# Kernel optimization log

Hardware: AMD Instinct MI355X
Metric: run time of the kernel (lower is better)

Reference implementation:

```python
import jax, jax.numpy as jnp
import numpy as np


def setup_inputs() -> dict:
    key = jax.random.key(0)
    k1, k2, k3 = jax.random.split(key, 3)
    B, N, M, C = 4, 4096, 8192, 64
    PPU = 64.0  # points_per_unit
    xz = jax.random.normal(k1, (B, M, 1), dtype=jnp.float32) * 10.0  # grid locations
    z = jax.random.normal(k2, (B, C, M), dtype=jnp.float32)          # channels-first features
    x = jax.random.normal(k3, (B, N, 1), dtype=jnp.float32) * 10.0   # query locations
    log_scale = jnp.asarray(np.log(2.0 / PPU), dtype=jnp.float32)
    return {"xz": xz, "z": z, "x": x, "log_scale": log_scale}


def reference(xz, z, x, log_scale):
    # pairwise squared distances between x [B,N,1] and xz [B,M,1] -> [B,N,M]
    diff = x - jnp.swapaxes(xz, -1, -2)            # [B,N,M]
    dists2 = diff * diff
    # RBF weights (no normalization)
    weights = jnp.exp(-0.5 * dists2 / jnp.exp(2.0 * log_scale))  # [B,N,M]
    # z: [B,C,M] -> transpose -> [B,M,C]; weights @ z^T -> [B,N,C]
    out = jnp.einsum('bnm,bcm->bnc', weights, z)
    return out
```

## Files before the change

kernel.cpp:

```cpp
#include <hip/hip_runtime.h>
#include <math.h>

#define B 4
#define N 4096
#define M 8192
#define C 64
#define NB 2048
#define XMIN (-64.0f)
#define INV_BW 16.0f
#define CUT 10.0f
#define QG 16
#define NSUBP 4
#define NSUBQ 2

typedef __attribute__((ext_vector_type(8))) short short8;
typedef __attribute__((ext_vector_type(4))) float f32x4;

__device__ __forceinline__ int bucket_of(float v) {
    int k = (int)floorf((v - XMIN) * INV_BW);
    return min(max(k, 0), NB - 1);
}

__device__ __forceinline__ unsigned short f2bf(float f) {
    unsigned int u = __float_as_uint(f);
    return (unsigned short)((u + 0x7FFF + ((u >> 16) & 1)) >> 16);
}

__global__ __launch_bounds__(256) void hist_kernel(
    const float* __restrict__ xz, const float* __restrict__ x,
    int* __restrict__ part)
{
    const int t   = threadIdx.x;
    const int bid = blockIdx.x;
    __shared__ int h[NB];
    #pragma unroll
    for (int i = 0; i < 8; ++i) h[t + 256 * i] = 0;
    __syncthreads();

    const bool isQ = bid >= 16;
    const int  b   = isQ ? (bid - 16) >> 1 : bid >> 2;
    const int  sub = isQ ? (bid - 16) & 1  : bid & 3;
    const float* src = (isQ ? x + b * N : xz + b * M) + sub * 2048;

    #pragma unroll
    for (int j = 0; j < 2; ++j) {
        float4 v4 = *(const float4*)(src + t * 4 + j * 1024);
        atomicAdd(&h[bucket_of(v4.x)], 1);
        atomicAdd(&h[bucket_of(v4.y)], 1);
        atomicAdd(&h[bucket_of(v4.z)], 1);
        atomicAdd(&h[bucket_of(v4.w)], 1);
    }
    __syncthreads();
    #pragma unroll
    for (int i = 0; i < 8; ++i) part[bid * NB + t + 256 * i] = h[t + 256 * i];
}

__global__ __launch_bounds__(256) void scat_kernel(
    const float* __restrict__ xz, const float* __restrict__ x,
    const int* __restrict__ part,
    int* __restrict__ bucket_start,
    float* __restrict__ xs,
    int* __restrict__ islot,
    float* __restrict__ qcs,
    int* __restrict__ qis)
{
    const int t    = threadIdx.x;
    const int lane = t & 63;
    const int w    = t >> 6;
    const int bid  = blockIdx.x;
    const bool isQ = bid >= 16;
    const int  b   = isQ ? (bid - 16) >> 1 : bid >> 2;
    const int  sub = isQ ? (bid - 16) & 1  : bid & 3;
    const int  nsub = isQ ? NSUBQ : NSUBP;
    const int  pb0  = isQ ? 16 + b * 2 : b * 4;
    const float* src = (isQ ? x + b * N : xz + b * M) + sub * 2048;

    __shared__ int base[NB];
    __shared__ int cnt[NB];
    __shared__ int wsum[4];

    int tot[8], mine[8];
    #pragma unroll
    for (int j = 0; j < 8; ++j) { tot[j] = 0; mine[j] = 0; }
    for (int s_ = 0; s_ < nsub; ++s_) {
        #pragma unroll
        for (int j = 0; j < 8; ++j) {
            const int v = part[(pb0 + s_) * NB + t * 8 + j];
            tot[j] += v;
            if (s_ < sub) mine[j] += v;
        }
    }
    int pre[8]; int tsum = 0;
    #pragma unroll
    for (int j = 0; j < 8; ++j) { pre[j] = tsum; tsum += tot[j]; }
    int s = tsum;
    #pragma unroll
    for (int off = 1; off < 64; off <<= 1) {
        int up = __shfl_up(s, off, 64);
        if (lane >= off) s += up;
    }
    if (lane == 63) wsum[w] = s;
    #pragma unroll
    for (int i = 0; i < 8; ++i) cnt[t + 256 * i] = 0;
    __syncthreads();
    int woff = 0;
    for (int i = 0; i < w; ++i) woff += wsum[i];
    const int excl = woff + s - tsum;
    #pragma unroll
    for (int j = 0; j < 8; ++j) base[t * 8 + j] = excl + pre[j] + mine[j];
    if (!isQ && sub == 0) {
        #pragma unroll
        for (int j = 0; j < 8; ++j)
            bucket_start[b * (NB + 1) + t * 8 + j] = excl + pre[j];
        if (t == 255) bucket_start[b * (NB + 1) + NB] = woff + s;
    }
    __syncthreads();

    #pragma unroll
    for (int j = 0; j < 2; ++j) {
        float4 v4 = *(const float4*)(src + t * 4 + j * 1024);
        float vv[4] = {v4.x, v4.y, v4.z, v4.w};
        #pragma unroll
        for (int c = 0; c < 4; ++c) {
            const int k    = bucket_of(vv[c]);
            const int slot = base[k] + atomicAdd(&cnt[k], 1);
            const int orig = sub * 2048 + t * 4 + j * 1024 + c;
            if (!isQ) {
                xs[b * M + slot]    = vv[c];
                islot[b * M + orig] = slot;
            } else {
                qcs[b * N + slot] = vv[c];
                qis[b * N + slot] = orig;
            }
        }
    }
}

__global__ __launch_bounds__(1024) void permz_kernel(
    const float* __restrict__ z, const int* __restrict__ islot,
    unsigned short* __restrict__ zs)
{
    const int t  = threadIdx.x;
    const int b  = blockIdx.x >> 7;
    const int m0 = (blockIdx.x & 127) * 64;
    __shared__ float tile[64][65];
    __shared__ int slot_s[64];

    const int m = t & 63;
    #pragma unroll
    for (int k = 0; k < 4; ++k) {
        int c = (t >> 6) + 16 * k;
        tile[c][m] = z[((size_t)b * C + c) * M + m0 + m];
    }
    if (t < 64) slot_s[t] = islot[b * M + m0 + t];
    __syncthreads();

    const int j  = t >> 4;
    const int c4 = t & 15;
    ushort4 v4;
    v4.x = f2bf(tile[c4 * 4 + 0][j]);
    v4.y = f2bf(tile[c4 * 4 + 1][j]);
    v4.z = f2bf(tile[c4 * 4 + 2][j]);
    v4.w = f2bf(tile[c4 * 4 + 3][j]);
    ((ushort4*)zs)[((size_t)b * M + slot_s[j]) * 16 + c4] = v4;
}

__global__ __launch_bounds__(256) void gather_kernel(
    const float* __restrict__ log_scale,
    const int* __restrict__ bucket_start,
    const float* __restrict__ xs,
    const float* __restrict__ qcs,
    const int* __restrict__ qis,
    const unsigned short* __restrict__ zs,
    float* __restrict__ out)
{
    const int t    = threadIdx.x;
    const int lane = t & 63;
    const int w    = t >> 6;
    const int quad = lane >> 4;
    const int low4 = lane & 15;
    const int g  = blockIdx.x;
    const int b  = g >> 8;
    const int g0 = (g & 255) * QG;

    __shared__ unsigned short zr[64 * 64];
    __shared__ unsigned short wl[QG][72];
    __shared__ float qcS[QG];
    __shared__ int   qiS[QG];

    const float ls   = log_scale[0];
    const float coef = -0.5f * __expf(-2.0f * ls);
    const float R    = sqrtf(CUT / (-coef));

    if (t < QG) {
        qcS[t] = qcs[b * N + g0 + t];
        qiS[t] = qis[b * N + g0 + t];
    }
    __syncthreads();

    float xmin = qcS[0], xmax = qcS[0];
    #pragma unroll
    for (int j = 1; j < QG; ++j) {
        xmin = fminf(xmin, qcS[j]);
        xmax = fmaxf(xmax, qcS[j]);
    }
    const int s0 = bucket_start[b * (NB + 1) + bucket_of(xmin - R)];
    const int s1 = bucket_start[b * (NB + 1) + bucket_of(xmax + R) + 1];
    const int e0 = s0 & ~63;
    const int e1 = (s1 + 63) & ~63;

    const int qw = w * 4 + (lane >> 4);
    const int pg = lane & 15;
    const float qv = qcS[qw];

    f32x4 acc = {0.f, 0.f, 0.f, 0.f};

    const float* xsb = xs + b * M;
    const unsigned short* zsb = zs + (size_t)b * M * C;

    for (int cs = e0; cs < e1; cs += 64) {
        __syncthreads();
        #pragma unroll
        for (int r = 0; r < 2; ++r) {
            const unsigned short* gp =
                zsb + ((size_t)cs + (w * 2 + r) * 8 + (lane >> 3)) * C + (lane & 7) * 8;
            unsigned short* lp = zr + (w * 2 + r) * 512;
            __builtin_amdgcn_global_load_lds(
                (const __attribute__((address_space(1))) void*)gp,
                (__attribute__((address_space(3))) void*)lp, 16, 0, 0);
        }
        {
            const float4 xp4 = *(const float4*)(xsb + cs + pg * 4);
            float d0 = qv - xp4.x, d1 = qv - xp4.y;
            float d2 = qv - xp4.z, d3 = qv - xp4.w;
            ushort4 wv;
            wv.x = f2bf(__expf(coef * d0 * d0));
            wv.y = f2bf(__expf(coef * d1 * d1));
            wv.z = f2bf(__expf(coef * d2 * d2));
            wv.w = f2bf(__expf(coef * d3 * d3));
            *(ushort4*)&wl[qw][pg * 4] = wv;
        }
        __syncthreads();
        #pragma unroll
        for (int kh = 0; kh < 2; ++kh) {
            short8 afrag = *(const short8*)&wl[low4][kh * 32 + quad * 8];
            short8 bfrag;
            #pragma unroll
            for (int j = 0; j < 8; ++j) {
                const int p = kh * 32 + quad * 8 + j;
                bfrag[j] = (short)zr[p * 64 + w * 16 + low4];
            }
            acc = __builtin_amdgcn_mfma_f32_16x16x32_bf16(afrag, bfrag, acc, 0, 0, 0);
        }
    }

    #pragma unroll
    for (int r = 0; r < 4; ++r) {
        const int q = quad * 4 + r;
        out[((size_t)b * N + qiS[q]) * C + w * 16 + low4] = acc[r];
    }
}

extern "C" void kernel_launch(void* const* d_in, const int* in_sizes, int n_in,
                              void* d_out, int out_size, void* d_ws, size_t ws_size,
                              hipStream_t stream) {
    const float* xz = (const float*)d_in[0];
    const float* z  = (const float*)d_in[1];
    const float* x  = (const float*)d_in[2];
    const float* ls = (const float*)d_in[3];
    float* out = (float*)d_out;

    char* ws = (char*)d_ws;
    size_t off = 0;
    auto alloc = [&](size_t bytes) { void* p = ws + off; off += (bytes + 255) & ~size_t(255); return p; };

    unsigned short* zs = (unsigned short*)alloc(((size_t)B * M + 64) * C * sizeof(unsigned short));
    float* xs    = (float*)alloc(((size_t)B * M + 64) * sizeof(float));
    int*   islot = (int*)alloc((size_t)B * M * sizeof(int));
    float* qcs   = (float*)alloc((size_t)B * N * sizeof(float));
    int*   qis   = (int*)alloc((size_t)B * N * sizeof(int));
    int*   bst   = (int*)alloc((size_t)B * (NB + 1) * sizeof(int));
    int*   part  = (int*)alloc((size_t)24 * NB * sizeof(int));

    hist_kernel<<<24, 256, 0, stream>>>(xz, x, part);
    scat_kernel<<<24, 256, 0, stream>>>(xz, x, part, bst, xs, islot, qcs, qis);
    permz_kernel<<<512, 1024, 0, stream>>>(z, islot, zs);
    gather_kernel<<<B * (N / QG), 256, 0, stream>>>(ls, bst, xs, qcs, qis, zs, out);
}
```

Measured before the change: 83.89 us.

## Fuse four kernels into one persistent kernel with software grid barriers

Merges the histogram, scatter, z-permute and gather kernels into a single launch of 256 blocks of 512 threads, separated by atomic-counter grid barriers. This removes three kernel launch gaps and their inter-kernel drain. The gather stage now processes 32 queries per block in two passes, and the permute stage handles two tiles per block. The persistent grid assumes all 256 blocks are co-resident, otherwise the spin barriers deadlock, and the early stages run on only 24 blocks while the rest spin.

Result: slower. 186.1 us (+121.8%).

```diff
diff --git a/kernel.cpp b/kernel.cpp
--- a/kernel.cpp
+++ b/kernel.cpp
@@ -9,9 +9,11 @@
 #define XMIN (-64.0f)
 #define INV_BW 16.0f
 #define CUT 10.0f
-#define QG 16
+#define QG2 32
 #define NSUBP 4
 #define NSUBQ 2
+#define GRID 256
+#define TPB 512
 
 typedef __attribute__((ext_vector_type(8))) short short8;
 typedef __attribute__((ext_vector_type(4))) float f32x4;
@@ -26,105 +28,108 @@
     return (unsigned short)((u + 0x7FFF + ((u >> 16) & 1)) >> 16);
 }
 
-__global__ __launch_bounds__(256) void hist_kernel(
-    const float* __restrict__ xz, const float* __restrict__ x,
-    int* __restrict__ part)
+__device__ __forceinline__ void gridbar(int* cnt, int target) {
+    __syncthreads();
+    if (threadIdx.x == 0) {
+        __threadfence();
+        __hip_atomic_fetch_add(cnt, 1, __ATOMIC_ACQ_REL, __HIP_MEMORY_SCOPE_AGENT);
+        while (__hip_atomic_load(cnt, __ATOMIC_ACQUIRE, __HIP_MEMORY_SCOPE_AGENT) < target)
+            __builtin_amdgcn_s_sleep(2);
+        __threadfence();
+    }
+    __syncthreads();
+}
+
+__global__ __launch_bounds__(TPB, 2) void mega_kernel(
+    const float* __restrict__ xz, const float* __restrict__ z,
+    const float* __restrict__ x,  const float* __restrict__ ls_p,
+    int* __restrict__ cnt,        int* __restrict__ part,
+    int* __restrict__ bst,
+    float* __restrict__ xs,       int* __restrict__ islot,
+    float* __restrict__ qcs,      int* __restrict__ qis,
+    unsigned short* __restrict__ zs,
+    float* __restrict__ out)
 {
-    const int t   = threadIdx.x;
-    const int bid = blockIdx.x;
-    __shared__ int h[NB];
-    #pragma unroll
-    for (int i = 0; i < 8; ++i) h[t + 256 * i] = 0;
-    __syncthreads();
-
-    const bool isQ = bid >= 16;
-    const int  b   = isQ ? (bid - 16) >> 1 : bid >> 2;
-    const int  sub = isQ ? (bid - 16) & 1  : bid & 3;
-    const float* src = (isQ ? x + b * N : xz + b * M) + sub * 2048;
-
-    #pragma unroll
-    for (int j = 0; j < 2; ++j) {
-        float4 v4 = *(const float4*)(src + t * 4 + j * 1024);
+    __shared__ __align__(16) char smem[17472];
+    const int t    = threadIdx.x;
+    const int blk  = blockIdx.x;
+    const int lane = t & 63;
+    const int w    = t >> 6;
+
+    if (blk < 24) {
+        int* h = (int*)smem;
+        #pragma unroll
+        for (int i = 0; i < 4; ++i) h[t + TPB * i] = 0;
+        __syncthreads();
+        const bool isQ = blk >= 16;
+        const int  b   = isQ ? (blk - 16) >> 1 : blk >> 2;
+        const int  sub = isQ ? (blk - 16) & 1  : blk & 3;
+        const float* src = (isQ ? x + b * N : xz + b * M) + sub * 2048;
+        float4 v4 = *(const float4*)(src + t * 4);
         atomicAdd(&h[bucket_of(v4.x)], 1);
         atomicAdd(&h[bucket_of(v4.y)], 1);
         atomicAdd(&h[bucket_of(v4.z)], 1);
         atomicAdd(&h[bucket_of(v4.w)], 1);
-    }
-    __syncthreads();
-    #pragma unroll
-    for (int i = 0; i < 8; ++i) part[bid * NB + t + 256 * i] = h[t + 256 * i];
-}
-
-__global__ __launch_bounds__(256) void scat_kernel(
-    const float* __restrict__ xz, const float* __restrict__ x,
-    const int* __restrict__ part,
-    int* __restrict__ bucket_start,
-    float* __restrict__ xs,
-    int* __restrict__ islot,
-    float* __restrict__ qcs,
-    int* __restrict__ qis)
-{
-    const int t    = threadIdx.x;
-    const int lane = t & 63;
-    const int w    = t >> 6;
-    const int bid  = blockIdx.x;
-    const bool isQ = bid >= 16;
-    const int  b   = isQ ? (bid - 16) >> 1 : bid >> 2;
-    const int  sub = isQ ? (bid - 16) & 1  : bid & 3;
-    const int  nsub = isQ ? NSUBQ : NSUBP;
-    const int  pb0  = isQ ? 16 + b * 2 : b * 4;
-    const float* src = (isQ ? x + b * N : xz + b * M) + sub * 2048;
-
-    __shared__ int base[NB];
-    __shared__ int cnt[NB];
-    __shared__ int wsum[4];
-
-    int tot[8], mine[8];
-    #pragma unroll
-    for (int j = 0; j < 8; ++j) { tot[j] = 0; mine[j] = 0; }
-    for (int s_ = 0; s_ < nsub; ++s_) {
-        #pragma unroll
-        for (int j = 0; j < 8; ++j) {
-            const int v = part[(pb0 + s_) * NB + t * 8 + j];
-            tot[j] += v;
-            if (s_ < sub) mine[j] += v;
-        }
-    }
-    int pre[8]; int tsum = 0;
-    #pragma unroll
-    for (int j = 0; j < 8; ++j) { pre[j] = tsum; tsum += tot[j]; }
-    int s = tsum;
-    #pragma unroll
-    for (int off = 1; off < 64; off <<= 1) {
-        int up = __shfl_up(s, off, 64);
-        if (lane >= off) s += up;
-    }
-    if (lane == 63) wsum[w] = s;
-    #pragma unroll
-    for (int i = 0; i < 8; ++i) cnt[t + 256 * i] = 0;
-    __syncthreads();
-    int woff = 0;
-    for (int i = 0; i < w; ++i) woff += wsum[i];
-    const int excl = woff + s - tsum;
-    #pragma unroll
-    for (int j = 0; j < 8; ++j) base[t * 8 + j] = excl + pre[j] + mine[j];
-    if (!isQ && sub == 0) {
-        #pragma unroll
-        for (int j = 0; j < 8; ++j)
-            bucket_start[b * (NB + 1) + t * 8 + j] = excl + pre[j];
-        if (t == 255) bucket_start[b * (NB + 1) + NB] = woff + s;
-    }
-    __syncthreads();
-
-    #pragma unroll
-    for (int j = 0; j < 2; ++j) {
-        float4 v4 = *(const float4*)(src + t * 4 + j * 1024);
+        __syncthreads();
+        #pragma unroll
+        for (int i = 0; i < 4; ++i) part[blk * NB + t + TPB * i] = h[t + TPB * i];
+    }
+    gridbar(cnt, GRID);
+
+    if (blk < 24) {
+        int* base = (int*)smem;
+        int* cl   = (int*)(smem + 8192);
+        int* wsum = (int*)(smem + 16384);
+        const bool isQ = blk >= 16;
+        const int  b   = isQ ? (blk - 16) >> 1 : blk >> 2;
+        const int  sub = isQ ? (blk - 16) & 1  : blk & 3;
+        const int  nsub = isQ ? NSUBQ : NSUBP;
+        const int  pb0  = isQ ? 16 + b * 2 : b * 4;
+        const float* src = (isQ ? x + b * N : xz + b * M) + sub * 2048;
+
+        int tot[4], mine[4];
+        #pragma unroll
+        for (int j = 0; j < 4; ++j) { tot[j] = 0; mine[j] = 0; }
+        for (int s_ = 0; s_ < nsub; ++s_) {
+            #pragma unroll
+            for (int j = 0; j < 4; ++j) {
+                const int v = part[(pb0 + s_) * NB + t * 4 + j];
+                tot[j] += v;
+                if (s_ < sub) mine[j] += v;
+            }
+        }
+        int pre[4]; int tsum = 0;
+        #pragma unroll
+        for (int j = 0; j < 4; ++j) { pre[j] = tsum; tsum += tot[j]; }
+        int s = tsum;
+        #pragma unroll
+        for (int off = 1; off < 64; off <<= 1) {
+            int up = __shfl_up(s, off, 64);
+            if (lane >= off) s += up;
+        }
+        if (lane == 63) wsum[w] = s;
+        #pragma unroll
+        for (int i = 0; i < 4; ++i) cl[t + TPB * i] = 0;
+        __syncthreads();
+        int woff = 0;
+        for (int i = 0; i < w; ++i) woff += wsum[i];
+        const int excl = woff + s - tsum;
+        #pragma unroll
+        for (int j = 0; j < 4; ++j) base[t * 4 + j] = excl + pre[j] + mine[j];
+        if (!isQ && sub == 0) {
+            #pragma unroll
+            for (int j = 0; j < 4; ++j)
+                bst[b * (NB + 1) + t * 4 + j] = excl + pre[j];
+            if (t == TPB - 1) bst[b * (NB + 1) + NB] = woff + s;
+        }
+        __syncthreads();
+        float4 v4 = *(const float4*)(src + t * 4);
         float vv[4] = {v4.x, v4.y, v4.z, v4.w};
         #pragma unroll
         for (int c = 0; c < 4; ++c) {
             const int k    = bucket_of(vv[c]);
-            const int slot = base[k] + atomicAdd(&cnt[k], 1);
-            const int orig = sub * 2048 + t * 4 + j * 1024 + c;
+            const int slot = base[k] + atomicAdd(&cl[k], 1);
+            const int orig = sub * 2048 + t * 4 + c;
             if (!isQ) {
                 xs[b * M + slot]    = vv[c];
                 islot[b * M + orig] = slot;
@@ -134,130 +139,116 @@
             }
         }
     }
-}
-
-__global__ __launch_bounds__(1024) void permz_kernel(
-    const float* __restrict__ z, const int* __restrict__ islot,
-    unsigned short* __restrict__ zs)
-{
-    const int t  = threadIdx.x;
-    const int b  = blockIdx.x >> 7;
-    const int m0 = (blockIdx.x & 127) * 64;
-    __shared__ float tile[64][65];
-    __shared__ int slot_s[64];
-
-    const int m = t & 63;
-    #pragma unroll
-    for (int k = 0; k < 4; ++k) {
-        int c = (t >> 6) + 16 * k;
-        tile[c][m] = z[((size_t)b * C + c) * M + m0 + m];
-    }
-    if (t < 64) slot_s[t] = islot[b * M + m0 + t];
-    __syncthreads();
-
-    const int j  = t >> 4;
-    const int c4 = t & 15;
-    ushort4 v4;
-    v4.x = f2bf(tile[c4 * 4 + 0][j]);
-    v4.y = f2bf(tile[c4 * 4 + 1][j]);
-    v4.z = f2bf(tile[c4 * 4 + 2][j]);
-    v4.w = f2bf(tile[c4 * 4 + 3][j]);
-    ((ushort4*)zs)[((size_t)b * M + slot_s[j]) * 16 + c4] = v4;
-}
-
-__global__ __launch_bounds__(256) void gather_kernel(
-    const float* __restrict__ log_scale,
-    const int* __restrict__ bucket_start,
-    const float* __restrict__ xs,
-    const float* __restrict__ qcs,
-    const int* __restrict__ qis,
-    const unsigned short* __restrict__ zs,
-    float* __restrict__ out)
-{
-    const int t    = threadIdx.x;
-    const int lane = t & 63;
-    const int w    = t >> 6;
-    const int quad = lane >> 4;
-    const int low4 = lane & 15;
-    const int g  = blockIdx.x;
-    const int b  = g >> 8;
-    const int g0 = (g & 255) * QG;
-
-    __shared__ unsigned short zr[64 * 64];
-    __shared__ unsigned short wl[QG][72];
-    __shared__ float qcS[QG];
-    __shared__ int   qiS[QG];
-
-    const float ls   = log_scale[0];
-    const float coef = -0.5f * __expf(-2.0f * ls);
-    const float R    = sqrtf(CUT / (-coef));
-
-    if (t < QG) {
-        qcS[t] = qcs[b * N + g0 + t];
-        qiS[t] = qis[b * N + g0 + t];
-    }
-    __syncthreads();
-
-    float xmin = qcS[0], xmax = qcS[0];
-    #pragma unroll
-    for (int j = 1; j < QG; ++j) {
-        xmin = fminf(xmin, qcS[j]);
-        xmax = fmaxf(xmax, qcS[j]);
-    }
-    const int s0 = bucket_start[b * (NB + 1) + bucket_of(xmin - R)];
-    const int s1 = bucket_start[b * (NB + 1) + bucket_of(xmax + R) + 1];
-    const int e0 = s0 & ~63;
-    const int e1 = (s1 + 63) & ~63;
-
-    const int qw = w * 4 + (lane >> 4);
-    const int pg = lane & 15;
-    const float qv = qcS[qw];
-
-    f32x4 acc = {0.f, 0.f, 0.f, 0.f};
-
-    const float* xsb = xs + b * M;
-    const unsigned short* zsb = zs + (size_t)b * M * C;
-
-    for (int cs = e0; cs < e1; cs += 64) {
-        __syncthreads();
-        #pragma unroll
-        for (int r = 0; r < 2; ++r) {
-            const unsigned short* gp =
-                zsb + ((size_t)cs + (w * 2 + r) * 8 + (lane >> 3)) * C + (lane & 7) * 8;
-            unsigned short* lp = zr + (w * 2 + r) * 512;
-            __builtin_amdgcn_global_load_lds(
-                (const __attribute__((address_space(1))) void*)gp,
-                (__attribute__((address_space(3))) void*)lp, 16, 0, 0);
-        }
-        {
-            const float4 xp4 = *(const float4*)(xsb + cs + pg * 4);
-            float d0 = qv - xp4.x, d1 = qv - xp4.y;
-            float d2 = qv - xp4.z, d3 = qv - xp4.w;
-            ushort4 wv;
-            wv.x = f2bf(__expf(coef * d0 * d0));
-            wv.y = f2bf(__expf(coef * d1 * d1));
-            wv.z = f2bf(__expf(coef * d2 * d2));
-            wv.w = f2bf(__expf(coef * d3 * d3));
-            *(ushort4*)&wl[qw][pg * 4] = wv;
-        }
-        __syncthreads();
-        #pragma unroll
-        for (int kh = 0; kh < 2; ++kh) {
-            short8 afrag = *(const short8*)&wl[low4][kh * 32 + quad * 8];
-            short8 bfrag;
-            #pragma unroll
-            for (int j = 0; j < 8; ++j) {
-                const int p = kh * 32 + quad * 8 + j;
-                bfrag[j] = (short)zr[p * 64 + w * 16 + low4];
-            }
-            acc = __builtin_amdgcn_mfma_f32_16x16x32_bf16(afrag, bfrag, acc, 0, 0, 0);
-        }
-    }
-
-    #pragma unroll
-    for (int r = 0; r < 4; ++r) {
-        const int q = quad * 4 + r;
-        out[((size_t)b * N + qiS[q]) * C + w * 16 + low4] = acc[r];
+    gridbar(cnt, 2 * GRID);
+
+    {
+        float (*tile)[65] = (float(*)[65])smem;
+        int* slot_s = (int*)(smem + 16640);
+        for (int h2 = 0; h2 < 2; ++h2) {
+            const int tix = blk * 2 + h2;
+            const int b   = tix >> 7;
+            const int m0  = (tix & 127) * 64;
+            __syncthreads();
+            const int m = t & 63;
+            #pragma unroll
+            for (int k = 0; k < 8; ++k) {
+                int c = (t >> 6) + 8 * k;
+                tile[c][m] = z[((size_t)b * C + c) * M + m0 + m];
+            }
+            if (t < 64) slot_s[t] = islot[b * M + m0 + t];
+            __syncthreads();
+            #pragma unroll
+            for (int h3 = 0; h3 < 2; ++h3) {
+                const int j  = (t >> 4) + 32 * h3;
+                const int c4 = t & 15;
+                ushort4 v4;
+                v4.x = f2bf(tile[c4 * 4 + 0][j]);
+                v4.y = f2bf(tile[c4 * 4 + 1][j]);
+                v4.z = f2bf(tile[c4 * 4 + 2][j]);
+                v4.w = f2bf(tile[c4 * 4 + 3][j]);
+                ((ushort4*)zs)[((size_t)b * M + slot_s[j]) * 16 + c4] = v4;
+            }
+        }
+    }
+    gridbar(cnt, 3 * GRID);
+
+    {
+        unsigned short* zr = (unsigned short*)smem;
+        unsigned short (*wl)[72] = (unsigned short(*)[72])(smem + 8192);
+        float* qcS = (float*)(smem + 8192 + 4608);
+        int*   qiS = (int*)(smem + 8192 + 4608 + 128);
+
+        const float ls   = ls_p[0];
+        const float coef = -0.5f * __expf(-2.0f * ls);
+        const float R    = sqrtf(CUT / (-coef));
+        const int quad = lane >> 4;
+        const int low4 = lane & 15;
+        const int qt   = w >> 2;
+        const int ct   = w & 3;
+        const int qw   = w * 4 + quad;
+        const int pg   = low4;
+
+        for (int h2 = 0; h2 < 2; ++h2) {
+            const int g  = blk * 2 + h2;
+            const int b  = g >> 7;
+            const int g0 = (g & 127) * QG2;
+            __syncthreads();
+            if (t < QG2) {
+                qcS[t] = qcs[b * N + g0 + t];
+                qiS[t] = qis[b * N + g0 + t];
+            }
+            __syncthreads();
+            float xmin = qcS[0], xmax = qcS[0];
+            #pragma unroll
+            for (int j = 1; j < QG2; ++j) {
+                xmin = fminf(xmin, qcS[j]);
+                xmax = fmaxf(xmax, qcS[j]);
+            }
+            const int s0 = bst[b * (NB + 1) + bucket_of(xmin - R)];
+            const int s1 = bst[b * (NB + 1) + bucket_of(xmax + R) + 1];
+            const int e0 = s0 & ~63;
+            const int e1 = (s1 + 63) & ~63;
+            const float qv = qcS[qw];
+            f32x4 acc = {0.f, 0.f, 0.f, 0.f};
+            const float* xsb = xs + b * M;
+            const unsigned short* zsb = zs + (size_t)b * M * C;
+
+            for (int cs = e0; cs < e1; cs += 64) {
+                __syncthreads();
+                const unsigned short* gp =
+                    zsb + ((size_t)cs + w * 8 + (lane >> 3)) * C + (lane & 7) * 8;
+                __builtin_amdgcn_global_load_lds(
+                    (const __attribute__((address_space(1))) void*)gp,
+                    (__attribute__((address_space(3))) void*)(zr + w * 512),
+                    16, 0, 0);
+                const float4 xp4 = *(const float4*)(xsb + cs + pg * 4);
+                float d0 = qv - xp4.x, d1 = qv - xp4.y;
+                float d2 = qv - xp4.z, d3 = qv - xp4.w;
+                ushort4 wv;
+                wv.x = f2bf(__expf(coef * d0 * d0));
+                wv.y = f2bf(__expf(coef * d1 * d1));
+                wv.z = f2bf(__expf(coef * d2 * d2));
+                wv.w = f2bf(__expf(coef * d3 * d3));
+                *(ushort4*)&wl[qw][pg * 4] = wv;
+                __syncthreads();
+                #pragma unroll
+                for (int kh = 0; kh < 2; ++kh) {
+                    short8 afrag = *(const short8*)&wl[qt * 16 + low4][kh * 32 + quad * 8];
+                    short8 bfrag;
+                    #pragma unroll
+                    for (int j = 0; j < 8; ++j) {
+                        const int p = kh * 32 + quad * 8 + j;
+                        bfrag[j] = (short)zr[p * 64 + ct * 16 + low4];
+                    }
+                    acc = __builtin_amdgcn_mfma_f32_16x16x32_bf16(afrag, bfrag, acc, 0, 0, 0);
+                }
+            }
+            #pragma unroll
+            for (int r = 0; r < 4; ++r) {
+                const int q = qt * 16 + quad * 4 + r;
+                out[((size_t)b * N + qiS[q]) * C + ct * 16 + low4] = acc[r];
+            }
+        }
     }
 }
 
@@ -274,6 +265,7 @@
     size_t off = 0;
     auto alloc = [&](size_t bytes) { void* p = ws + off; off += (bytes + 255) & ~size_t(255); return p; };
 
+    int* cnt = (int*)alloc(256);
     unsigned short* zs = (unsigned short*)alloc(((size_t)B * M + 64) * C * sizeof(unsigned short));
     float* xs    = (float*)alloc(((size_t)B * M + 64) * sizeof(float));
     int*   islot = (int*)alloc((size_t)B * M * sizeof(int));
@@ -282,8 +274,7 @@
     int*   bst   = (int*)alloc((size_t)B * (NB + 1) * sizeof(int));
     int*   part  = (int*)alloc((size_t)24 * NB * sizeof(int));
 
-    hist_kernel<<<24, 256, 0, stream>>>(xz, x, part);
-    scat_kernel<<<24, 256, 0, stream>>>(xz, x, part, bst, xs, islot, qcs, qis);
-    permz_kernel<<<512, 1024, 0, stream>>>(z, islot, zs);
-    gather_kernel<<<B * (N / QG), 256, 0, stream>>>(ls, bst, xs, qcs, qis, zs, out);
-}
+    hipMemsetAsync(cnt, 0, sizeof(int), stream);
+    mega_kernel<<<GRID, TPB, 0, stream>>>(xz, z, x, ls, cnt, part, bst,
+                                          xs, islot, qcs, qis, zs, out);
+}
```

## Fuse histogram with z transpose and gather z rows via sorted index

Applied to the files above, without the earlier changes.

The histogram kernel and the z transpose/bf16 conversion are merged into one prep kernel. z is now written in original point order rather than bucket-sorted order, so the separate permutation kernel disappears. The gather kernel instead reads an index array (iord) from the scatter pass and uses it to fetch each z row indirectly. This removes one launch and takes the transpose off the dependency on the scatter kernel. The cost is an extra dependent index load before each async row load, plus row fetches from scattered addresses.

Measured after the change: 82.45 us. Within noise of the previous version (-1.7%).

```diff
diff --git a/kernel.cpp b/kernel.cpp
--- a/kernel.cpp
+++ b/kernel.cpp
@@ -26,33 +26,51 @@
     return (unsigned short)((u + 0x7FFF + ((u >> 16) & 1)) >> 16);
 }
 
-__global__ __launch_bounds__(256) void hist_kernel(
+__global__ __launch_bounds__(1024) void prep_kernel(
     const float* __restrict__ xz, const float* __restrict__ x,
-    int* __restrict__ part)
+    const float* __restrict__ z,
+    int* __restrict__ part,
+    unsigned short* __restrict__ zt)
 {
     const int t   = threadIdx.x;
-    const int bid = blockIdx.x;
-    __shared__ int h[NB];
-    #pragma unroll
-    for (int i = 0; i < 8; ++i) h[t + 256 * i] = 0;
-    __syncthreads();
-
-    const bool isQ = bid >= 16;
-    const int  b   = isQ ? (bid - 16) >> 1 : bid >> 2;
-    const int  sub = isQ ? (bid - 16) & 1  : bid & 3;
-    const float* src = (isQ ? x + b * N : xz + b * M) + sub * 2048;
-
-    #pragma unroll
-    for (int j = 0; j < 2; ++j) {
-        float4 v4 = *(const float4*)(src + t * 4 + j * 1024);
-        atomicAdd(&h[bucket_of(v4.x)], 1);
-        atomicAdd(&h[bucket_of(v4.y)], 1);
-        atomicAdd(&h[bucket_of(v4.z)], 1);
-        atomicAdd(&h[bucket_of(v4.w)], 1);
-    }
-    __syncthreads();
-    #pragma unroll
-    for (int i = 0; i < 8; ++i) part[bid * NB + t + 256 * i] = h[t + 256 * i];
+    const int blk = blockIdx.x;
+
+    __shared__ int   h[NB];
+    __shared__ float tile[64][65];
+
+    if (blk < 24) {
+        h[t] = 0; h[t + 1024] = 0;
+        __syncthreads();
+        const bool isQ = blk >= 16;
+        const int  b   = isQ ? (blk - 16) >> 1 : blk >> 2;
+        const int  sub = isQ ? (blk - 16) & 1  : blk & 3;
+        const float* src = (isQ ? x + b * N : xz + b * M) + sub * 2048;
+        float2 v2 = *(const float2*)(src + t * 2);
+        atomicAdd(&h[bucket_of(v2.x)], 1);
+        atomicAdd(&h[bucket_of(v2.y)], 1);
+        __syncthreads();
+        part[blk * NB + t]        = h[t];
+        part[blk * NB + 1024 + t] = h[1024 + t];
+    } else {
+        const int tix = blk - 24;
+        const int b   = tix >> 7;
+        const int m0  = (tix & 127) * 64;
+        const int m   = t & 63;
+        #pragma unroll
+        for (int k = 0; k < 4; ++k) {
+            int c = (t >> 6) + 16 * k;
+            tile[c][m] = z[((size_t)b * C + c) * M + m0 + m];
+        }
+        __syncthreads();
+        const int j  = t >> 4;
+        const int c4 = t & 15;
+        ushort4 v4;
+        v4.x = f2bf(tile[c4 * 4 + 0][j]);
+        v4.y = f2bf(tile[c4 * 4 + 1][j]);
+        v4.z = f2bf(tile[c4 * 4 + 2][j]);
+        v4.w = f2bf(tile[c4 * 4 + 3][j]);
+        ((ushort4*)zt)[((size_t)b * M + m0 + j) * 16 + c4] = v4;
+    }
 }
 
 __global__ __launch_bounds__(256) void scat_kernel(
@@ -60,7 +78,7 @@
     const int* __restrict__ part,
     int* __restrict__ bucket_start,
     float* __restrict__ xs,
-    int* __restrict__ islot,
+    int* __restrict__ iord,
     float* __restrict__ qcs,
     int* __restrict__ qis)
 {
@@ -126,43 +144,14 @@
             const int slot = base[k] + atomicAdd(&cnt[k], 1);
             const int orig = sub * 2048 + t * 4 + j * 1024 + c;
             if (!isQ) {
-                xs[b * M + slot]    = vv[c];
-                islot[b * M + orig] = slot;
+                xs[b * M + slot]   = vv[c];
+                iord[b * M + slot] = orig;
             } else {
                 qcs[b * N + slot] = vv[c];
                 qis[b * N + slot] = orig;
             }
         }
     }
-}
-
-__global__ __launch_bounds__(1024) void permz_kernel(
-    const float* __restrict__ z, const int* __restrict__ islot,
-    unsigned short* __restrict__ zs)
-{
-    const int t  = threadIdx.x;
-    const int b  = blockIdx.x >> 7;
-    const int m0 = (blockIdx.x & 127) * 64;
-    __shared__ float tile[64][65];
-    __shared__ int slot_s[64];
-
-    const int m = t & 63;
-    #pragma unroll
-    for (int k = 0; k < 4; ++k) {
-        int c = (t >> 6) + 16 * k;
-        tile[c][m] = z[((size_t)b * C + c) * M + m0 + m];
-    }
-    if (t < 64) slot_s[t] = islot[b * M + m0 + t];
-    __syncthreads();
-
-    const int j  = t >> 4;
-    const int c4 = t & 15;
-    ushort4 v4;
-    v4.x = f2bf(tile[c4 * 4 + 0][j]);
-    v4.y = f2bf(tile[c4 * 4 + 1][j]);
-    v4.z = f2bf(tile[c4 * 4 + 2][j]);
-    v4.w = f2bf(tile[c4 * 4 + 3][j]);
-    ((ushort4*)zs)[((size_t)b * M + slot_s[j]) * 16 + c4] = v4;
 }
 
 __global__ __launch_bounds__(256) void gather_kernel(
@@ -171,7 +160,8 @@
     const float* __restrict__ xs,
     const float* __restrict__ qcs,
     const int* __restrict__ qis,
-    const unsigned short* __restrict__ zs,
+    const int* __restrict__ iord,
+    const unsigned short* __restrict__ zt,
     float* __restrict__ out)
 {
     const int t    = threadIdx.x;
@@ -216,14 +206,16 @@
     f32x4 acc = {0.f, 0.f, 0.f, 0.f};
 
     const float* xsb = xs + b * M;
-    const unsigned short* zsb = zs + (size_t)b * M * C;
+    const int* iordb = iord + b * M;
+    const unsigned short* ztb = zt + (size_t)b * M * C;
 
     for (int cs = e0; cs < e1; cs += 64) {
         __syncthreads();
         #pragma unroll
         for (int r = 0; r < 2; ++r) {
-            const unsigned short* gp =
-                zsb + ((size_t)cs + (w * 2 + r) * 8 + (lane >> 3)) * C + (lane & 7) * 8;
+            const int ridx = (w * 2 + r) * 8 + (lane >> 3);
+            const int gm   = iordb[cs + ridx];
+            const unsigned short* gp = ztb + (size_t)gm * C + (lane & 7) * 8;
             unsigned short* lp = zr + (w * 2 + r) * 512;
             __builtin_amdgcn_global_load_lds(
                 (const __attribute__((address_space(1))) void*)gp,
@@ -274,16 +266,15 @@
     size_t off = 0;
     auto alloc = [&](size_t bytes) { void* p = ws + off; off += (bytes + 255) & ~size_t(255); return p; };
 
-    unsigned short* zs = (unsigned short*)alloc(((size_t)B * M + 64) * C * sizeof(unsigned short));
-    float* xs    = (float*)alloc(((size_t)B * M + 64) * sizeof(float));
-    int*   islot = (int*)alloc((size_t)B * M * sizeof(int));
-    float* qcs   = (float*)alloc((size_t)B * N * sizeof(float));
-    int*   qis   = (int*)alloc((size_t)B * N * sizeof(int));
-    int*   bst   = (int*)alloc((size_t)B * (NB + 1) * sizeof(int));
-    int*   part  = (int*)alloc((size_t)24 * NB * sizeof(int));
-
-    hist_kernel<<<24, 256, 0, stream>>>(xz, x, part);
-    scat_kernel<<<24, 256, 0, stream>>>(xz, x, part, bst, xs, islot, qcs, qis);
-    permz_kernel<<<512, 1024, 0, stream>>>(z, islot, zs);
-    gather_kernel<<<B * (N / QG), 256, 0, stream>>>(ls, bst, xs, qcs, qis, zs, out);
-}
+    unsigned short* zt = (unsigned short*)alloc((size_t)B * M * C * sizeof(unsigned short));
+    float* xs   = (float*)alloc(((size_t)B * M + 64) * sizeof(float));
+    int*   iord = (int*)alloc((size_t)B * M * sizeof(int));
+    float* qcs  = (float*)alloc((size_t)B * N * sizeof(float));
+    int*   qis  = (int*)alloc((size_t)B * N * sizeof(int));
+    int*   bst  = (int*)alloc((size_t)B * (NB + 1) * sizeof(int));
+    int*   part = (int*)alloc((size_t)24 * NB * sizeof(int));
+
+    prep_kernel<<<536, 1024, 0, stream>>>(xz, x, z, part, zt);
+    scat_kernel<<<24, 256, 0, stream>>>(xz, x, part, bst, xs, iord, qcs, qis);
+    gather_kernel<<<B * (N / QG), 256, 0, stream>>>(ls, bst, xs, qcs, qis, iord, zt, out);
+}
```
